# Kernel tuning notes

Hardware: AMD Instinct MI355X
Metric: run time of the kernel (lower is better)

Reference implementation:

```python
import jax, jax.numpy as jnp
import numpy as np

D, H, N, K = 1024, 2048, 8, 2
B, S = 4, 2048

def setup_inputs() -> dict:
    key = jax.random.key(0)
    ks = jax.random.split(key, 4)
    x = jax.random.normal(ks[0], (B, S, D), dtype=jnp.float32)
    Wr = jax.random.normal(ks[1], (N, D), dtype=jnp.float32) / np.sqrt(D)
    br = jnp.zeros((N,), jnp.float32)
    Wl1 = jax.random.normal(ks[2], (N, D, 2 * H), dtype=jnp.float32) / np.sqrt(D)
    bl1 = jnp.zeros((N, 2 * H), jnp.float32)
    Wl2 = jax.random.normal(ks[3], (N, H, D), dtype=jnp.float32) / np.sqrt(H)
    bl2 = jnp.zeros((N, D), jnp.float32)
    biases_N = jnp.zeros((N,), jnp.float32)
    return {"x": x, "Wr": Wr, "br": br, "Wl1": Wl1, "bl1": bl1,
            "Wl2": Wl2, "bl2": bl2, "biases_N": biases_N}

def reference(x, Wr, br, Wl1, bl1, Wl2, bl2, biases_N):
    Bb, Ss, Dd = x.shape
    # router: Linear(D, N)
    scores_BSN = jnp.einsum('bsd,nd->bsn', x, Wr) + br
    w_BSN = jax.nn.softmax(scores_BSN, axis=-1)
    _, idx_BSK = jax.lax.top_k(scores_BSN + biases_N[None, None, :], K)
    val_BSK = jnp.take_along_axis(w_BSN, idx_BSK, axis=-1)
    val_BSK = val_BSK / jnp.sum(val_BSK, axis=-1, keepdims=True)

    M = Bb * Ss
    x_MD = x.reshape(M, Dd)
    idx_MK = idx_BSK.reshape(M, K)
    val_MK = val_BSK.reshape(M, K)

    # dense all-expert SwiGLU: h_NM2H -> silu(a)*b -> y_NMD
    h_NM2H = jnp.einsum('md,ndh->nmh', x_MD, Wl1) + bl1[:, None, :]
    a_NMH, b_NMH = h_NM2H[..., :H], h_NM2H[..., H:]
    y_NMD = jnp.einsum('nmh,nhd->nmd', jax.nn.silu(a_NMH) * b_NMH, Wl2) + bl2[:, None, :]

    # scatter top-k weights into dense [M, N] then weighted combine
    ew_MN = jnp.zeros((M, N), x.dtype)
    ew_MN = ew_MN.at[jnp.arange(M)[:, None], idx_MK].set(val_MK)
    y_MD = jnp.einsum('mn,nmd->md', ew_MN, y_NMD)
    return y_MD.reshape(Bb, Ss, Dd)
```

## Files before the change

### kernel.cpp

```cpp
#include <hip/hip_runtime.h>
#include <hip/hip_bf16.h>

#define D_ 1024
#define H_ 2048
#define H2_ 4096
#define NE 8
#define M_ 8192
#define RBMAX 72

typedef short v8s __attribute__((ext_vector_type(8)));
typedef float v4f __attribute__((ext_vector_type(4)));

typedef const __attribute__((address_space(1))) void gvoid_t;
typedef __attribute__((address_space(3))) void svoid_t;

__device__ __forceinline__ unsigned short f2b(float f) {
    __hip_bfloat16 h = __float2bfloat16(f);
    unsigned short u;
    __builtin_memcpy(&u, &h, sizeof(u));
    return u;
}

__global__ __launch_bounds__(256) void router_score_kernel(
    const float* __restrict__ x, const float* __restrict__ Wr,
    const float* __restrict__ br, const float* __restrict__ biases,
    int* __restrict__ pick, float* __restrict__ slot_w,
    unsigned short* __restrict__ xb) {
    int wid = threadIdx.x >> 6;
    int lane = threadIdx.x & 63;
    int m = blockIdx.x * 4 + wid;
    if (m >= M_) return;
    const float4* xr = (const float4*)(x + (size_t)m * D_);
    float4 xv[4];
#pragma unroll
    for (int p = 0; p < 4; ++p) xv[p] = xr[p * 64 + lane];
    ushort4* xbr = (ushort4*)(xb + (size_t)m * D_);
#pragma unroll
    for (int p = 0; p < 4; ++p) {
        ushort4 o;
        o.x = f2b(xv[p].x); o.y = f2b(xv[p].y); o.z = f2b(xv[p].z); o.w = f2b(xv[p].w);
        xbr[p * 64 + lane] = o;
    }
    float s[NE];
#pragma unroll
    for (int n = 0; n < NE; ++n) {
        const float4* wr = (const float4*)(Wr + (size_t)n * D_);
        float acc = 0.f;
#pragma unroll
        for (int p = 0; p < 4; ++p) {
            float4 w4 = wr[p * 64 + lane];
            acc += xv[p].x * w4.x + xv[p].y * w4.y + xv[p].z * w4.z + xv[p].w * w4.w;
        }
#pragma unroll
        for (int off = 32; off; off >>= 1) acc += __shfl_xor(acc, off, 64);
        s[n] = acc + br[n];
    }
    if (lane == 0) {
        float t[NE];
#pragma unroll
        for (int n = 0; n < NE; ++n) t[n] = s[n] + biases[n];
        int i0 = 0;
#pragma unroll
        for (int n = 1; n < NE; ++n) if (t[n] > t[i0]) i0 = n;
        int i1 = -1;
#pragma unroll
        for (int n = 0; n < NE; ++n) {
            if (n == i0) continue;
            if (i1 < 0 || t[n] > t[i1]) i1 = n;
        }
        float mx = fmaxf(s[i0], s[i1]);
        float e0 = expf(s[i0] - mx), e1 = expf(s[i1] - mx);
        float inv = 1.f / (e0 + e1);
        pick[m] = i0 | (i1 << 4);
        slot_w[m * 2] = e0 * inv;
        slot_w[m * 2 + 1] = e1 * inv;
    }
}

__global__ __launch_bounds__(256) void hist_kernel(const int* __restrict__ pick,
                                                   int* __restrict__ blkcnt) {
    __shared__ int h[NE];
    int t = threadIdx.x;
    if (t < NE) h[t] = 0;
    __syncthreads();
    int idx = blockIdx.x * 256 + t;
    int e = (pick[idx >> 1] >> ((idx & 1) * 4)) & 15;
    atomicAdd(&h[e], 1);
    __syncthreads();
    if (t < NE) blkcnt[blockIdx.x * NE + t] = h[t];
}

__global__ void scan_kernel(const int* __restrict__ blkcnt, int* __restrict__ blkoff,
                            int* __restrict__ cnt, int* __restrict__ bp) {
    int e = threadIdx.x;
    if (e < NE) {
        int run = 0;
        for (int b = 0; b < 64; ++b) {
            blkoff[b * NE + e] = run;
            run += blkcnt[b * NE + e];
        }
        cnt[e] = run;
    }
    __syncthreads();
    if (e == 0) {
        int b = 0, r = 0;
        for (int n = 0; n < NE; ++n) {
            bp[n] = b; bp[16 + n] = r;
            b += ((cnt[n] + 255) / 256) * 256;
            r += cnt[n];
        }
        bp[NE] = b; bp[16 + NE] = r;
    }
}

__global__ __launch_bounds__(256) void scatter_kernel(
    const int* __restrict__ pick, const int* __restrict__ blkoff,
    int* __restrict__ perm, int* __restrict__ slot_idx) {
    __shared__ int wvcnt[4 * NE];
    int t = threadIdx.x, lane = t & 63, w = t >> 6;
    int idx = blockIdx.x * 256 + t;
    int m = idx >> 1, sl = idx & 1;
    int e = (pick[m] >> (sl * 4)) & 15;
    unsigned long long ltm = (1ull << lane) - 1;
    int my = 0;
#pragma unroll
    for (int ee = 0; ee < NE; ++ee) {
        unsigned long long mask = __ballot(e == ee);
        if (ee == e) my = __popcll(mask & ltm);
        if (lane == ee) wvcnt[w * NE + ee] = __popcll(mask);
    }
    __syncthreads();
    int off = blkoff[blockIdx.x * NE + e] + my;
    for (int w2 = 0; w2 < w; ++w2) off += wvcnt[w2 * NE + e];
    perm[e * M_ + off] = m;
    slot_idx[m * 2 + sl] = (e << 13) | off;
}

__global__ __launch_bounds__(256) void pack_w1_kernel(const float* __restrict__ Wl1,
                                                      unsigned short* __restrict__ W1P) {
    int jb = blockIdx.x, t = blockIdx.y, e = blockIdx.z;
    int tid = threadIdx.x;
    int lr = tid;
    int q = lr >> 7;
    int h = jb * 128 + (tid & 127);
    size_t srcb = ((size_t)e * D_ + t * 64) * H2_ + (size_t)q * H_ + h;
    unsigned short* dst = W1P + ((((size_t)(e * 16 + jb) * 16 + t) * 2 + q) << 13) + ((lr & 127) * 8) * 8;
    int sw = lr & 7;
    v8s v;
#pragma unroll 2
    for (int g = 0; g < 8; ++g) {
#pragma unroll
        for (int j = 0; j < 8; ++j) {
            float f = Wl1[srcb + (size_t)(g * 8 + j) * H2_];
            v[j] = (short)f2b(f);
        }
        *(v8s*)(dst + (size_t)(g ^ sw) * 8) = v;
    }
}

__global__ __launch_bounds__(256) void pack_w2_kernel(const float* __restrict__ Wl2,
                                                      unsigned short* __restrict__ W2P) {
    int jb = blockIdx.x, t = blockIdx.y, e = blockIdx.z;
    int tid = threadIdx.x;
    int row = tid & 127, half = tid >> 7;
    int col = jb * 128 + row;
    unsigned short* dst = W2P + ((size_t)(e * 8 + jb) * 32 + t) * 8192 + row * 64;
#pragma unroll
    for (int gg = 0; gg < 4; ++gg) {
        int g = half * 4 + gg;
        int kgrp = g ^ (row & 7);
        v8s v;
#pragma unroll
        for (int j = 0; j < 8; ++j) {
            float f = Wl2[((size_t)e * H_ + t * 64 + kgrp * 8 + j) * D_ + col];
            v[j] = (short)f2b(f);
        }
        *(v8s*)(dst + g * 8) = v;
    }
}

#define GLDS(src, dst) __builtin_amdgcn_global_load_lds((gvoid_t*)(src), (svoid_t*)(dst), 16, 0, 0)
#define STB_(dstbase, t, q) { const unsigned short* s_ = Bsrc + (((size_t)(t) * 2 + (q)) << 13) + tid * 8; \
    GLDS(s_, (dstbase) + (q) * 8192 + tid * 8); \
    GLDS(s_ + 4096, (dstbase) + (q) * 8192 + 4096 + tid * 8); }
#define STA_X(dstbase, t, q) { \
    GLDS(aptr[q][0] + (size_t)(t) * 64, (dstbase) + (q) * 8192 + tid * 8); \
    GLDS(aptr[q][1] + (size_t)(t) * 64, (dstbase) + (q) * 8192 + 4096 + tid * 8); }

#define PHASE(Ab, Bb, QM, QN, LA, LB, STAGE_STMT, VM4) do { \
    if (LA) { _Pragma("unroll") for (int i_ = 0; i_ < 4; ++i_) { \
        const unsigned short* ar_ = (Ab) + ((QM) * 128 + wm * 64 + i_ * 16 + fr) * 64; \
        a_[i_][0] = *(const v8s*)(ar_ + s0); a_[i_][1] = *(const v8s*)(ar_ + s1); } } \
    if (LB) { _Pragma("unroll") for (int n_ = 0; n_ < 2; ++n_) { \
        const unsigned short* br_ = (Bb) + ((QN) * 128 + wn * 32 + n_ * 16 + fr) * 64; \
        b_[n_][0] = *(const v8s*)(br_ + s0); b_[n_][1] = *(const v8s*)(br_ + s1); } } \
    STAGE_STMT; \
    __builtin_amdgcn_sched_barrier(0); \
    __builtin_amdgcn_s_barrier(); \
    __builtin_amdgcn_s_setprio(1); \
    _Pragma("unroll") for (int kk_ = 0; kk_ < 2; ++kk_) \
        _Pragma("unroll") for (int i_ = 0; i_ < 4; ++i_) \
            _Pragma("unroll") for (int n_ = 0; n_ < 2; ++n_) \
                acc[(QM) * 4 + i_][(QN) * 2 + n_] = __builtin_amdgcn_mfma_f32_16x16x32_bf16( \
                    a_[i_][kk_], b_[n_][kk_], acc[(QM) * 4 + i_][(QN) * 2 + n_], 0, 0, 0); \
    __builtin_amdgcn_s_setprio(0); \
    __builtin_amdgcn_sched_barrier(0); \
    if (VM4) { asm volatile("s_waitcnt vmcnt(4)" ::: "memory"); } \
    __builtin_amdgcn_s_barrier(); \
} while (0)

__global__ __launch_bounds__(512, 2) void gemm1_kernel(
    const unsigned short* __restrict__ xb, const unsigned short* __restrict__ Bpack,
    const float* __restrict__ bias, const int* __restrict__ cnt, const int* __restrict__ bp,
    const int* __restrict__ perm, unsigned short* __restrict__ actP) {
    constexpr int NT = 16;
    int p = blockIdx.x;
    int tm = (p >> 3) & 31;
    int pid = (p & 7) + ((p >> 8) << 3);
    int e = pid >> 4;
    int jb = pid & 15;
    int cn = cnt[e];
    if (tm * 256 >= cn) return;
    int rb = (bp[e] >> 8) + tm;

    __shared__ __align__(16) unsigned short SH[66560];
    unsigned short* As0 = SH;
    unsigned short* As1 = SH + 16384;
    unsigned short* Bs0 = SH + 32768;
    unsigned short* Bs1 = SH + 49152;

    int tid = threadIdx.x, lane = tid & 63, wid = tid >> 6;
    int wm = wid >> 2, wn = wid & 3;
    int fr = lane & 15, fg = lane >> 4;
    int swz = fr & 7;
    int s0 = (fg ^ swz) * 8;
    int s1 = ((4 + fg) ^ swz) * 8;

    int kgs = tid & 7;
    const unsigned short* aptr[2][2];
#pragma unroll
    for (int q = 0; q < 2; ++q)
#pragma unroll
        for (int h = 0; h < 2; ++h) {
            int lr = q * 128 + h * 64 + (tid >> 3);
            int r = ((lr >> 6) & 1) * 128 + ((lr >> 7) & 1) * 64 + (lr & 63);
            int rl = min(tm * 256 + r, cn - 1);
            int tok = perm[e * M_ + rl];
            aptr[q][h] = xb + (size_t)tok * D_ + ((kgs ^ (lr & 7)) << 3);
        }

    const unsigned short* Bsrc = Bpack + (((size_t)(e * 16 + jb) * NT) << 14);

    v4f acc[8][4] = {};
    v8s a_[4][2];
    v8s b_[2][2];

    STA_X(As0, 0, 0); STB_(Bs0, 0, 1); STA_X(As0, 0, 1); STB_(Bs0, 0, 0);
    STA_X(As1, 1, 0); STB_(Bs1, 1, 1);
    asm volatile("s_waitcnt vmcnt(0)" ::: "memory");
    __builtin_amdgcn_s_barrier();

    for (int i2 = 0; i2 < NT / 2; ++i2) {
        int T1 = 2 * i2 + 1;
        int T2c = min(2 * i2 + 2, NT - 1);
        int T3c = min(2 * i2 + 3, NT - 1);
        PHASE(As0, Bs0, 0, 0, 1, 1, STA_X(As1, T1, 1), 0);
        PHASE(As0, Bs0, 0, 1, 0, 1, STB_(Bs1, T1, 0), 0);
        PHASE(As0, Bs0, 1, 1, 1, 0, STA_X(As0, T2c, 0), 0);
        PHASE(As0, Bs0, 1, 0, 0, 1, STB_(Bs0, T2c, 1), 1);
        PHASE(As1, Bs1, 0, 0, 1, 1, STA_X(As0, T2c, 1), 0);
        PHASE(As1, Bs1, 0, 1, 0, 1, STB_(Bs0, T2c, 0), 0);
        PHASE(As1, Bs1, 1, 1, 1, 0, STA_X(As1, T3c, 0), 0);
        PHASE(As1, Bs1, 1, 0, 0, 1, STB_(Bs1, T3c, 1), 1);
    }
    asm volatile("s_waitcnt vmcnt(0)" ::: "memory");
    __syncthreads();

    unsigned short* actl = SH;
    int hl0 = wn * 32 + fr, hl1 = wn * 32 + 16 + fr;
    float ba0 = bias[e * H2_ + jb * 128 + hl0];
    float bb0 = bias[e * H2_ + H_ + jb * 128 + hl0];
    float ba1 = bias[e * H2_ + jb * 128 + hl1];
    float bb1 = bias[e * H2_ + H_ + jb * 128 + hl1];
#pragma unroll
    for (int I = 0; I < 8; ++I) {
        int r0 = wm * 128 + (I >> 2) * 64 + (I & 3) * 16 + fg * 4;
#pragma unroll
        for (int rr = 0; rr < 4; ++rr) {
            float a0 = acc[I][0][rr] + ba0, b0 = acc[I][2][rr] + bb0;
            float a1 = acc[I][1][rr] + ba1, b1 = acc[I][3][rr] + bb1;
            actl[(r0 + rr) * 136 + hl0] = f2b(a0 / (1.f + __expf(-a0)) * b0);
            actl[(r0 + rr) * 136 + hl1] = f2b(a1 / (1.f + __expf(-a1)) * b1);
        }
    }
    __syncthreads();
#pragma unroll
    for (int c8 = 0; c8 < 8; ++c8) {
        int cid = c8 * 512 + tid;
        int t2l = cid >> 11, rem = cid & 2047;
        int q = rem >> 10, s = rem & 1023;
        int lr = q * 128 + (s >> 3);
        int g = (s & 7) ^ (lr & 7);
        int r = ((lr >> 6) & 1) * 128 + (lr >> 7) * 64 + (lr & 63);
        v8s v = *(const v8s*)(actl + r * 136 + t2l * 64 + g * 8);
        *(v8s*)(actP + ((((size_t)rb * 32 + jb * 2 + t2l) * 2 + q) << 13) + s * 8) = v;
    }
}

#define STAH2(dst, t, q) { const unsigned short* s_ = Asrc + (((size_t)(t) * 2 + (q)) << 13) + tid * 8; \
    GLDS(s_, (dst) + (q) * 8192 + tid * 8); \
    GLDS(s_ + 4096, (dst) + (q) * 8192 + 4096 + tid * 8); }
#define STBH2(dst, t, h) { const unsigned short* s_ = Bsrc + ((size_t)(t) * 8192) + (h) * 4096 + tid * 8; \
    GLDS(s_, (dst) + (h) * 4096 + tid * 8); }

#define PHASE2(Ab, Bp_, QM, LB, STAGE_STMT) do { \
    _Pragma("unroll") for (int i_ = 0; i_ < 4; ++i_) { \
        const unsigned short* ar_ = (Ab) + ((QM) * 128 + wm * 64 + i_ * 16 + fr) * 64; \
        a_[i_][0] = *(const v8s*)(ar_ + s0); a_[i_][1] = *(const v8s*)(ar_ + s1); } \
    if (LB) { _Pragma("unroll") for (int n_ = 0; n_ < 2; ++n_) { \
        const unsigned short* br_ = (Bp_) + (wn * 32 + n_ * 16 + fr) * 64; \
        b_[n_][0] = *(const v8s*)(br_ + s0); b_[n_][1] = *(const v8s*)(br_ + s1); } } \
    STAGE_STMT; \
    __builtin_amdgcn_sched_barrier(0); \
    __builtin_amdgcn_s_barrier(); \
    __builtin_amdgcn_s_setprio(1); \
    _Pragma("unroll") for (int kk_ = 0; kk_ < 2; ++kk_) \
        _Pragma("unroll") for (int i_ = 0; i_ < 4; ++i_) \
            _Pragma("unroll") for (int n_ = 0; n_ < 2; ++n_) \
                acc[(QM) * 4 + i_][n_] = __builtin_amdgcn_mfma_f32_16x16x32_bf16( \
                    a_[i_][kk_], b_[n_][kk_], acc[(QM) * 4 + i_][n_], 0, 0, 0); \
    __builtin_amdgcn_s_setprio(0); \
    __builtin_amdgcn_sched_barrier(0); \
    asm volatile("s_waitcnt vmcnt(6)" ::: "memory"); \
    __builtin_amdgcn_s_barrier(); \
} while (0)

__global__ __launch_bounds__(512, 2) void gemm2_kernel(
    const unsigned short* __restrict__ actP, const unsigned short* __restrict__ W2P,
    const float* __restrict__ bl2, const int* __restrict__ cnt, const int* __restrict__ bp,
    float* __restrict__ y) {
    constexpr int NT = 32;
    int p = blockIdx.x;
    int tm = (p >> 3) & 31;
    int pid = (p & 7) + ((p >> 8) << 3);
    int e = pid >> 3;
    int jb = pid & 7;
    int cn = cnt[e];
    if (tm * 256 >= cn) return;
    int rb = (bp[e] >> 8) + tm;

    __shared__ __align__(16) unsigned short SH[57344];
    unsigned short* As0 = SH;
    unsigned short* As1 = SH + 16384;
    unsigned short* Bb0 = SH + 32768;
    unsigned short* Bb1 = SH + 40960;
    unsigned short* Bb2 = SH + 49152;

    int tid = threadIdx.x, lane = tid & 63, wid = tid >> 6;
    int wm = wid >> 2, wn = wid & 3;
    int fr = lane & 15, fg = lane >> 4;
    int swz = fr & 7;
    int s0 = (fg ^ swz) * 8;
    int s1 = ((4 + fg) ^ swz) * 8;

    const unsigned short* Asrc = actP + ((size_t)rb << 19);
    const unsigned short* Bsrc = W2P + ((size_t)(e * 8 + jb) * 32) * 8192;

    v4f acc[8][2] = {};
    v8s a_[4][2];
    v8s b_[2][2];

    STAH2(As0, 0, 0); STAH2(As0, 0, 1);
    STBH2(Bb0, 0, 0); STBH2(Bb0, 0, 1);
    STAH2(As1, 1, 0);
    STBH2(Bb1, 1, 0); STBH2(Bb1, 1, 1);
    asm volatile("s_waitcnt vmcnt(0)" ::: "memory");
    __builtin_amdgcn_s_barrier();

    unsigned short* Bc0 = Bb0;
    unsigned short* Bc1 = Bb1;
    unsigned short* Bn = Bb2;
    for (int i2 = 0; i2 < NT / 2; ++i2) {
        int T1 = 2 * i2 + 1;
        int T2 = min(2 * i2 + 2, NT - 1);
        int T3 = min(2 * i2 + 3, NT - 1);
        PHASE2(As0, Bc0, 0, 1, { STAH2(As1, T1, 1); STBH2(Bn, T2, 0); });
        PHASE2(As0, Bc0, 1, 0, { STAH2(As0, T2, 0); STBH2(Bn, T2, 1); });
        PHASE2(As1, Bc1, 0, 1, { STAH2(As0, T2, 1); STBH2(Bc0, T3, 0); });
        PHASE2(As1, Bc1, 1, 0, { STAH2(As1, T3, 0); STBH2(Bc0, T3, 1); });
        unsigned short* oB0 = Bc0;
        Bc0 = Bn; Bn = Bc1; Bc1 = oB0;
    }
    asm volatile("s_waitcnt vmcnt(0)" ::: "memory");
    __syncthreads();

    float* yl = (float*)SH;
    int bsr = bp[16 + e];
    float b2_0 = bl2[e * D_ + jb * 128 + wn * 32 + fr];
    float b2_1 = bl2[e * D_ + jb * 128 + wn * 32 + 16 + fr];
#pragma unroll
    for (int wmp = 0; wmp < 2; ++wmp) {
        if (wm == wmp) {
#pragma unroll
            for (int I = 0; I < 8; ++I) {
                int r0 = (I >> 2) * 64 + (I & 3) * 16 + fg * 4;
#pragma unroll
                for (int rr = 0; rr < 4; ++rr) {
                    yl[(r0 + rr) * 132 + wn * 32 + fr] = acc[I][0][rr] + b2_0;
                    yl[(r0 + rr) * 132 + wn * 32 + 16 + fr] = acc[I][1][rr] + b2_1;
                }
            }
        }
        __syncthreads();
#pragma unroll
        for (int f = 0; f < 8; ++f) {
            int fid = f * 512 + tid;
            int row = fid >> 5, c4 = fid & 31;
            int rp = tm * 256 + wmp * 128 + row;
            if (rp < cn) {
                float4 v = *(const float4*)(yl + row * 132 + c4 * 4);
                *(float4*)(y + (size_t)(bsr + rp) * D_ + jb * 128 + c4 * 4) = v;
            }
        }
        __syncthreads();
    }
}

__global__ __launch_bounds__(256) void combine_kernel(
    const float* __restrict__ y, const int* __restrict__ slot_idx,
    const float* __restrict__ slot_w, const int* __restrict__ bp,
    float* __restrict__ out) {
    int m = blockIdx.x * 4 + (threadIdx.x >> 6);
    int t2 = threadIdx.x & 63;
    int i0 = slot_idx[m * 2], i1 = slot_idx[m * 2 + 1];
    float w0 = slot_w[m * 2], w1 = slot_w[m * 2 + 1];
    const float4* y0 = (const float4*)(y + (size_t)(bp[16 + (i0 >> 13)] + (i0 & (M_ - 1))) * D_);
    const float4* y1 = (const float4*)(y + (size_t)(bp[16 + (i1 >> 13)] + (i1 & (M_ - 1))) * D_);
    float4* o = (float4*)(out + (size_t)m * D_);
#pragma unroll
    for (int k = 0; k < 4; ++k) {
        int idx = k * 64 + t2;
        float4 a = y0[idx], b = y1[idx];
        float4 r;
        r.x = w0 * a.x + w1 * b.x;
        r.y = w0 * a.y + w1 * b.y;
        r.z = w0 * a.z + w1 * b.z;
        r.w = w0 * a.w + w1 * b.w;
        o[idx] = r;
    }
}

__global__ void ws_fail_kernel(float* __restrict__ out) {
    if (threadIdx.x == 0 && blockIdx.x == 0) out[0] = 1e30f;
}

extern "C" void kernel_launch(void* const* d_in, const int* in_sizes, int n_in,
                              void* d_out, int out_size, void* d_ws, size_t ws_size,
                              hipStream_t stream) {
    const float* x = (const float*)d_in[0];
    const float* Wr = (const float*)d_in[1];
    const float* br = (const float*)d_in[2];
    const float* Wl1 = (const float*)d_in[3];
    const float* bl1 = (const float*)d_in[4];
    const float* Wl2 = (const float*)d_in[5];
    const float* bl2 = (const float*)d_in[6];
    const float* biases = (const float*)d_in[7];
    float* out = (float*)d_out;

    char* ws = (char*)d_ws;
    size_t off = 0;
    auto alloc = [&](size_t bytes) {
        char* p = ws + off;
        off += (bytes + 255) & ~(size_t)255;
        return p;
    };
    unsigned short* W1P = (unsigned short*)alloc((size_t)NE * 16 * 16 * 2 * 8192 * 2);
    unsigned short* W2P = (unsigned short*)alloc((size_t)NE * 8 * 32 * 8192 * 2);
    unsigned short* xb = (unsigned short*)alloc((size_t)M_ * D_ * 2);
    unsigned short* actP = (unsigned short*)alloc((size_t)RBMAX * 32 * 2 * 8192 * 2);
    int* perm = (int*)alloc((size_t)NE * M_ * 4);
    int* slot_idx = (int*)alloc((size_t)M_ * 2 * 4);
    float* slot_w = (float*)alloc((size_t)M_ * 2 * 4);
    int* pick = (int*)alloc((size_t)M_ * 4);
    int* blkcnt = (int*)alloc(64 * NE * 4);
    int* blkoff = (int*)alloc(64 * NE * 4);
    int* cnt = (int*)alloc(256);
    int* bp = (int*)alloc(256);
    float* y = (float*)W1P;
    if (ws_size < off) {
        ws_fail_kernel<<<1, 64, 0, stream>>>(out);
        return;
    }

    pack_w1_kernel<<<dim3(16, 16, NE), 256, 0, stream>>>(Wl1, W1P);
    pack_w2_kernel<<<dim3(8, 32, NE), 256, 0, stream>>>(Wl2, W2P);
    router_score_kernel<<<M_ / 4, 256, 0, stream>>>(x, Wr, br, biases, pick, slot_w, xb);
    hist_kernel<<<64, 256, 0, stream>>>(pick, blkcnt);
    scan_kernel<<<1, 64, 0, stream>>>(blkcnt, blkoff, cnt, bp);
    scatter_kernel<<<64, 256, 0, stream>>>(pick, blkoff, perm, slot_idx);
    gemm1_kernel<<<32 * 16 * NE, 512, 0, stream>>>(xb, W1P, bl1, cnt, bp, perm, actP);
    gemm2_kernel<<<32 * 8 * NE, 512, 0, stream>>>(actP, W2P, bl2, cnt, bp, y);
    combine_kernel<<<M_ / 4, 256, 0, stream>>>(y, slot_idx, slot_w, bp, out);
}
```

Before: 407.4 us.

## Double-buffer MFMA register fragments to overlap LDS reads with compute

Both expert GEMM kernels now keep two sets of register fragments for A and B. Each phase loads the next phase's fragments from LDS while the MFMAs run on the current set, and the barrier before the MFMAs is removed, leaving one barrier per phase after a combined vmcnt/lgkmcnt wait. This is meant to hide LDS read latency behind matrix-core work and cut synchronisation. The costs are more VGPRs, which threatens occupancy at launch bounds (512,2), and a reordered stage/read schedule whose correctness depends on the wait counts lining up with buffer reuse.

```diff
diff --git a/kernel.cpp b/kernel.cpp
--- a/kernel.cpp
+++ b/kernel.cpp
@@ -187,27 +187,41 @@
     GLDS(aptr[q][0] + (size_t)(t) * 64, (dstbase) + (q) * 8192 + tid * 8); \
     GLDS(aptr[q][1] + (size_t)(t) * 64, (dstbase) + (q) * 8192 + 4096 + tid * 8); }
 
-#define PHASE(Ab, Bb, QM, QN, LA, LB, STAGE_STMT, VM4) do { \
-    if (LA) { _Pragma("unroll") for (int i_ = 0; i_ < 4; ++i_) { \
-        const unsigned short* ar_ = (Ab) + ((QM) * 128 + wm * 64 + i_ * 16 + fr) * 64; \
-        a_[i_][0] = *(const v8s*)(ar_ + s0); a_[i_][1] = *(const v8s*)(ar_ + s1); } } \
-    if (LB) { _Pragma("unroll") for (int n_ = 0; n_ < 2; ++n_) { \
-        const unsigned short* br_ = (Bb) + ((QN) * 128 + wn * 32 + n_ * 16 + fr) * 64; \
-        b_[n_][0] = *(const v8s*)(br_ + s0); b_[n_][1] = *(const v8s*)(br_ + s1); } } \
-    STAGE_STMT; \
+#define LDA1(DST, Ab, QM) { _Pragma("unroll") for (int i_ = 0; i_ < 4; ++i_) { \
+    const unsigned short* ar_ = (Ab) + ((QM) * 128 + wm * 64 + i_ * 16 + fr) * 64; \
+    DST[i_][0] = *(const v8s*)(ar_ + s0); DST[i_][1] = *(const v8s*)(ar_ + s1); } }
+#define LDB1(DST, Bb, QN) { _Pragma("unroll") for (int n_ = 0; n_ < 2; ++n_) { \
+    const unsigned short* br_ = (Bb) + ((QN) * 128 + wn * 32 + n_ * 16 + fr) * 64; \
+    DST[n_][0] = *(const v8s*)(br_ + s0); DST[n_][1] = *(const v8s*)(br_ + s1); } }
+#define LDB2(DST, Bp_) { _Pragma("unroll") for (int n_ = 0; n_ < 2; ++n_) { \
+    const unsigned short* br_ = (Bp_) + (wn * 32 + n_ * 16 + fr) * 64; \
+    DST[n_][0] = *(const v8s*)(br_ + s0); DST[n_][1] = *(const v8s*)(br_ + s1); } }
+
+#define MM1(AS, BS, QM, QN) \
     __builtin_amdgcn_sched_barrier(0); \
-    __builtin_amdgcn_s_barrier(); \
     __builtin_amdgcn_s_setprio(1); \
     _Pragma("unroll") for (int kk_ = 0; kk_ < 2; ++kk_) \
         _Pragma("unroll") for (int i_ = 0; i_ < 4; ++i_) \
             _Pragma("unroll") for (int n_ = 0; n_ < 2; ++n_) \
                 acc[(QM) * 4 + i_][(QN) * 2 + n_] = __builtin_amdgcn_mfma_f32_16x16x32_bf16( \
-                    a_[i_][kk_], b_[n_][kk_], acc[(QM) * 4 + i_][(QN) * 2 + n_], 0, 0, 0); \
+                    AS[i_][kk_], BS[n_][kk_], acc[(QM) * 4 + i_][(QN) * 2 + n_], 0, 0, 0); \
     __builtin_amdgcn_s_setprio(0); \
     __builtin_amdgcn_sched_barrier(0); \
-    if (VM4) { asm volatile("s_waitcnt vmcnt(4)" ::: "memory"); } \
-    __builtin_amdgcn_s_barrier(); \
-} while (0)
+    asm volatile("s_waitcnt vmcnt(4) lgkmcnt(0)" ::: "memory"); \
+    __builtin_amdgcn_s_barrier();
+
+#define MM2(AS, BS, QM) \
+    __builtin_amdgcn_sched_barrier(0); \
+    __builtin_amdgcn_s_setprio(1); \
+    _Pragma("unroll") for (int kk_ = 0; kk_ < 2; ++kk_) \
+        _Pragma("unroll") for (int i_ = 0; i_ < 4; ++i_) \
+            _Pragma("unroll") for (int n_ = 0; n_ < 2; ++n_) \
+                acc[(QM) * 4 + i_][n_] = __builtin_amdgcn_mfma_f32_16x16x32_bf16( \
+                    AS[i_][kk_], BS[n_][kk_], acc[(QM) * 4 + i_][n_], 0, 0, 0); \
+    __builtin_amdgcn_s_setprio(0); \
+    __builtin_amdgcn_sched_barrier(0); \
+    asm volatile("s_waitcnt vmcnt(3) lgkmcnt(0)" ::: "memory"); \
+    __builtin_amdgcn_s_barrier();
 
 __global__ __launch_bounds__(512, 2) void gemm1_kernel(
     const unsigned short* __restrict__ xb, const unsigned short* __restrict__ Bpack,
@@ -252,26 +266,27 @@
     const unsigned short* Bsrc = Bpack + (((size_t)(e * 16 + jb) * NT) << 14);
 
     v4f acc[8][4] = {};
-    v8s a_[4][2];
-    v8s b_[2][2];
+    v8s a0_[4][2], a1_[4][2];
+    v8s b0_[2][2], b1_[2][2];
 
     STA_X(As0, 0, 0); STB_(Bs0, 0, 1); STA_X(As0, 0, 1); STB_(Bs0, 0, 0);
     STA_X(As1, 1, 0); STB_(Bs1, 1, 1);
     asm volatile("s_waitcnt vmcnt(0)" ::: "memory");
     __builtin_amdgcn_s_barrier();
+    LDA1(a0_, As0, 0); LDB1(b0_, Bs0, 0);
 
     for (int i2 = 0; i2 < NT / 2; ++i2) {
         int T1 = 2 * i2 + 1;
         int T2c = min(2 * i2 + 2, NT - 1);
         int T3c = min(2 * i2 + 3, NT - 1);
-        PHASE(As0, Bs0, 0, 0, 1, 1, STA_X(As1, T1, 1), 0);
-        PHASE(As0, Bs0, 0, 1, 0, 1, STB_(Bs1, T1, 0), 0);
-        PHASE(As0, Bs0, 1, 1, 1, 0, STA_X(As0, T2c, 0), 0);
-        PHASE(As0, Bs0, 1, 0, 0, 1, STB_(Bs0, T2c, 1), 1);
-        PHASE(As1, Bs1, 0, 0, 1, 1, STA_X(As0, T2c, 1), 0);
-        PHASE(As1, Bs1, 0, 1, 0, 1, STB_(Bs0, T2c, 0), 0);
-        PHASE(As1, Bs1, 1, 1, 1, 0, STA_X(As1, T3c, 0), 0);
-        PHASE(As1, Bs1, 1, 0, 0, 1, STB_(Bs1, T3c, 1), 1);
+        LDB1(b1_, Bs0, 1); STB_(Bs1, T1, 0); MM1(a0_, b0_, 0, 0);
+        LDA1(a1_, As0, 1); STA_X(As1, T1, 1); MM1(a0_, b1_, 0, 1);
+        LDB1(b0_, Bs0, 0); STA_X(As0, T2c, 0); MM1(a1_, b1_, 1, 1);
+        LDA1(a0_, As1, 0); LDB1(b1_, Bs1, 0); STB_(Bs0, T2c, 1); MM1(a1_, b0_, 1, 0);
+        LDB1(b0_, Bs1, 1); STB_(Bs0, T2c, 0); MM1(a0_, b1_, 0, 0);
+        LDA1(a1_, As1, 1); STA_X(As0, T2c, 1); MM1(a0_, b0_, 0, 1);
+        LDB1(b1_, Bs1, 0); STA_X(As1, T3c, 0); MM1(a1_, b0_, 1, 1);
+        LDA1(a0_, As0, 0); LDB1(b0_, Bs0, 0); STB_(Bs1, T3c, 1); MM1(a1_, b1_, 1, 0);
     }
     asm volatile("s_waitcnt vmcnt(0)" ::: "memory");
     __syncthreads();
@@ -312,28 +327,6 @@
     GLDS(s_ + 4096, (dst) + (q) * 8192 + 4096 + tid * 8); }
 #define STBH2(dst, t, h) { const unsigned short* s_ = Bsrc + ((size_t)(t) * 8192) + (h) * 4096 + tid * 8; \
     GLDS(s_, (dst) + (h) * 4096 + tid * 8); }
-
-#define PHASE2(Ab, Bp_, QM, LB, STAGE_STMT) do { \
-    _Pragma("unroll") for (int i_ = 0; i_ < 4; ++i_) { \
-        const unsigned short* ar_ = (Ab) + ((QM) * 128 + wm * 64 + i_ * 16 + fr) * 64; \
-        a_[i_][0] = *(const v8s*)(ar_ + s0); a_[i_][1] = *(const v8s*)(ar_ + s1); } \
-    if (LB) { _Pragma("unroll") for (int n_ = 0; n_ < 2; ++n_) { \
-        const unsigned short* br_ = (Bp_) + (wn * 32 + n_ * 16 + fr) * 64; \
-        b_[n_][0] = *(const v8s*)(br_ + s0); b_[n_][1] = *(const v8s*)(br_ + s1); } } \
-    STAGE_STMT; \
-    __builtin_amdgcn_sched_barrier(0); \
-    __builtin_amdgcn_s_barrier(); \
-    __builtin_amdgcn_s_setprio(1); \
-    _Pragma("unroll") for (int kk_ = 0; kk_ < 2; ++kk_) \
-        _Pragma("unroll") for (int i_ = 0; i_ < 4; ++i_) \
-            _Pragma("unroll") for (int n_ = 0; n_ < 2; ++n_) \
-                acc[(QM) * 4 + i_][n_] = __builtin_amdgcn_mfma_f32_16x16x32_bf16( \
-                    a_[i_][kk_], b_[n_][kk_], acc[(QM) * 4 + i_][n_], 0, 0, 0); \
-    __builtin_amdgcn_s_setprio(0); \
-    __builtin_amdgcn_sched_barrier(0); \
-    asm volatile("s_waitcnt vmcnt(6)" ::: "memory"); \
-    __builtin_amdgcn_s_barrier(); \
-} while (0)
 
 __global__ __launch_bounds__(512, 2) void gemm2_kernel(
     const unsigned short* __restrict__ actP, const unsigned short* __restrict__ W2P,
@@ -367,8 +360,8 @@
     const unsigned short* Bsrc = W2P + ((size_t)(e * 8 + jb) * 32) * 8192;
 
     v4f acc[8][2] = {};
-    v8s a_[4][2];
-    v8s b_[2][2];
+    v8s a0_[4][2], a1_[4][2];
+    v8s b0_[2][2], b1_[2][2];
 
     STAH2(As0, 0, 0); STAH2(As0, 0, 1);
     STBH2(Bb0, 0, 0); STBH2(Bb0, 0, 1);
@@ -380,14 +373,16 @@
     unsigned short* Bc0 = Bb0;
     unsigned short* Bc1 = Bb1;
     unsigned short* Bn = Bb2;
+    LDA1(a0_, As0, 0); LDB2(b0_, Bc0);
+
     for (int i2 = 0; i2 < NT / 2; ++i2) {
         int T1 = 2 * i2 + 1;
         int T2 = min(2 * i2 + 2, NT - 1);
         int T3 = min(2 * i2 + 3, NT - 1);
-        PHASE2(As0, Bc0, 0, 1, { STAH2(As1, T1, 1); STBH2(Bn, T2, 0); });
-        PHASE2(As0, Bc0, 1, 0, { STAH2(As0, T2, 0); STBH2(Bn, T2, 1); });
-        PHASE2(As1, Bc1, 0, 1, { STAH2(As0, T2, 1); STBH2(Bc0, T3, 0); });
-        PHASE2(As1, Bc1, 1, 0, { STAH2(As1, T3, 0); STBH2(Bc0, T3, 1); });
+        LDA1(a1_, As0, 1); STAH2(As1, T1, 1); STBH2(Bn, T2, 0); MM2(a0_, b0_, 0);
+        LDA1(a0_, As1, 0); LDB2(b1_, Bc1); STAH2(As0, T2, 0); STBH2(Bn, T2, 1); MM2(a1_, b0_, 1);
+        LDA1(a1_, As1, 1); STAH2(As0, T2, 1); STBH2(Bc0, T3, 0); MM2(a0_, b1_, 0);
+        LDA1(a0_, As0, 0); LDB2(b0_, Bn); STAH2(As1, T3, 0); STBH2(Bc0, T3, 1); MM2(a1_, b1_, 1);
         unsigned short* oB0 = Bc0;
         Bc0 = Bn; Bn = Bc1; Bc1 = oB0;
     }
```

Result: slower. 533.5 us (+31.0%).
